# Performance work log

Measured on AMD Instinct MI355X. Metric: run time of the kernel, lower is better.

The kernel has to match this reference:

```python
import jax, jax.numpy as jnp
import numpy as np

N_HEAD = 12
NEG_BIG = 1e10  # additive mask constant from the source


def setup_inputs() -> dict:
    key = jax.random.key(0)
    k1, k2, k3 = jax.random.split(key, 3)
    B, S, D = 8, 1024, 768
    x = jax.random.normal(k1, (B, S, D), dtype=jnp.float32)
    W_attn = jax.random.normal(k2, (D, 3 * D), dtype=jnp.float32) * 0.02
    W_proj = jax.random.normal(k3, (D, D), dtype=jnp.float32) * 0.02
    return {"x": x, "W_attn": W_attn, "W_proj": W_proj}


def reference(x, W_attn, W_proj):
    B, S, D = x.shape
    H = N_HEAD
    dh = D // H  # head dim = 64

    c = x @ W_attn                       # [B, S, 3D]
    q, k, v = jnp.split(c, 3, axis=-1)   # each [B, S, D]

    def split_heads(t):
        return t.reshape(B, S, H, dh).transpose(0, 2, 1, 3)  # [B, H, S, dh]

    q, k, v = split_heads(q), split_heads(k), split_heads(v)

    scale = 1.0 / jnp.sqrt(jnp.asarray(dh, q.dtype))
    a = jnp.einsum('bhqd,bhkd->bhqk', q, k) * scale  # [B, H, S, S]

    # causal mask: i >= j - ns + nd with nd == ns -> lower triangular
    i = jnp.arange(S)[:, None]
    j = jnp.arange(S)[None, :]
    m = (i >= j).astype(a.dtype)  # [S, S]
    a = a * m - (1.0 - m) * NEG_BIG

    a = jax.nn.softmax(a, axis=-1)

    out = jnp.einsum('bhqk,bhkd->bhqd', a, v)        # [B, H, S, dh]
    out = out.transpose(0, 2, 1, 3).reshape(B, S, D)  # merge heads
    return out @ W_proj
```

## Files before the change

### kernel.cpp

```cpp
#include <hip/hip_runtime.h>
#include <hip/hip_bf16.h>

typedef __attribute__((ext_vector_type(4))) float f32x4;
typedef __attribute__((ext_vector_type(8))) short short8;
typedef unsigned short u16;
typedef unsigned int u32;

__device__ __forceinline__ u16 f2bf(float f) {
    u32 u = __float_as_uint(f);
    u32 r = (u + 0x7fffu + ((u >> 16) & 1u)) >> 16;
    return (u16)r;
}
__device__ __forceinline__ u32 pack2bf(float a, float b) {
    __hip_bfloat162 w = __float22bfloat162_rn(float2{a, b});
    return *(u32*)&w;
}
__device__ __forceinline__ void stage16(const u16* gsrc, u16* ldsdst) {
    __builtin_amdgcn_global_load_lds((const __attribute__((address_space(1))) void*)gsrc,
                                     (__attribute__((address_space(3))) void*)ldsdst, 16, 0, 0);
}

__global__ __launch_bounds__(256) void prep(const float* __restrict__ x,
                                            const float* __restrict__ Wa,
                                            const float* __restrict__ Wp,
                                            u16* __restrict__ xb, u16* __restrict__ wat,
                                            u16* __restrict__ wpt) {
    __shared__ float tile[64][65];
    int blk = blockIdx.x;
    if (blk < 576) {
        const float* W;
        u16* Wt;
        int N, bx, by;
        if (blk < 432) {
            W = Wa; Wt = wat; N = 2304; bx = blk % 36; by = blk / 36;
        } else {
            int i = blk - 432;
            W = Wp; Wt = wpt; N = 768; bx = i % 12; by = i / 12;
        }
        int n0 = bx * 64, k0 = by * 64;
        int c = threadIdx.x & 63, r0 = threadIdx.x >> 6;
#pragma unroll
        for (int i = 0; i < 16; ++i) {
            int r = r0 * 16 + i;
            tile[r][c] = W[(size_t)(k0 + r) * N + n0 + c];
        }
        __syncthreads();
#pragma unroll
        for (int i = 0; i < 16; ++i) {
            int r = r0 * 16 + i;
            Wt[(size_t)(n0 + r) * 768 + k0 + c] = f2bf(tile[c][r]);
        }
    } else {
        const int n4 = (8 * 1024 * 768) / 4;
        int i = (blk - 576) * 256 + threadIdx.x;
        int stride = 1024 * 256;
        for (; i < n4; i += stride) {
            float4 v = ((const float4*)x)[i];
            ushort4 o;
            o.x = f2bf(v.x); o.y = f2bf(v.y); o.z = f2bf(v.z); o.w = f2bf(v.w);
            ((ushort4*)xb)[i] = o;
        }
    }
}

template <int MODE, int WM>
__global__ __launch_bounds__(256, 4) void gemmT(const u16* __restrict__ A,
                                                const u16* __restrict__ Bt,
                                                u16* __restrict__ q, u16* __restrict__ kk,
                                                u16* __restrict__ v, float* __restrict__ outf,
                                                int nby) {
    const int K = 768;
    const int BM = 2 * WM;
    __shared__ __align__(16) u16 As[BM * 64];
    __shared__ __align__(16) u16 Bs[128 * 64];
    int nwg = gridDim.x;
    int bid = blockIdx.x;
    int wgid = (bid & 7) * (nwg >> 3) + (bid >> 3);
    int mb = wgid / nby, nb = wgid % nby;
    int m0 = mb * BM, n0 = nb * 128;
    int tid = threadIdx.x;
    int wave = tid >> 6, lane = tid & 63;
    int lo = lane & 15, hi = lane >> 4;
    int wm = (wave >> 1) * WM, wn = (wave & 1) * 64;
    int srow = lane >> 3;
    int schunk = (lane & 7) ^ srow;
    int sw0 = (hi ^ (lo & 7)) * 8;
    int sw1 = ((4 + hi) ^ (lo & 7)) * 8;
    f32x4 acc[WM / 16][4] = {};
    const u16* Ab = A + (size_t)(m0 + (BM / 4) * wave + srow) * K + schunk * 8;
    const u16* Bb = Bt + (size_t)(n0 + 32 * wave + srow) * K + schunk * 8;
    u16* ldsA = &As[((BM / 4) * wave) * 64];
    u16* ldsB = &Bs[(32 * wave) * 64];

    for (int k0 = 0; k0 < K; k0 += 64) {
#pragma unroll
        for (int c = 0; c < BM / 32; ++c)
            stage16(Ab + k0 + (size_t)(8 * c) * K, ldsA + c * 512);
#pragma unroll
        for (int c = 0; c < 4; ++c)
            stage16(Bb + k0 + (size_t)(8 * c) * K, ldsB + c * 512);
        __syncthreads();
#pragma unroll
        for (int ch = 0; ch < 2; ++ch) {
            int sw = ch ? sw1 : sw0;
            short8 af[WM / 16], bf[4];
#pragma unroll
            for (int i = 0; i < WM / 16; ++i)
                af[i] = *(const short8*)&As[(wm + 16 * i + lo) * 64 + sw];
#pragma unroll
            for (int j = 0; j < 4; ++j)
                bf[j] = *(const short8*)&Bs[(wn + 16 * j + lo) * 64 + sw];
#pragma unroll
            for (int i = 0; i < WM / 16; ++i)
#pragma unroll
                for (int j = 0; j < 4; ++j)
                    acc[i][j] = __builtin_amdgcn_mfma_f32_16x16x32_bf16(af[i], bf[j], acc[i][j], 0, 0, 0);
        }
        __syncthreads();
    }

    if (MODE == 0) {
        int ncb = n0 + wn;
        int which = ncb / 768;
        int h = (ncb % 768) >> 6;
        if (which == 2) {
#pragma unroll
            for (int i = 0; i < WM / 16; ++i) {
                int mrow = m0 + wm + 16 * i + 4 * hi;
                int b = mrow >> 10, s0 = mrow & 1023;
                size_t bh = (size_t)(b * 12 + h);
#pragma unroll
                for (int j = 0; j < 4; ++j) {
                    uint2 pk;
                    pk.x = pack2bf(acc[i][j][0], acc[i][j][1]);
                    pk.y = pack2bf(acc[i][j][2], acc[i][j][3]);
                    *(uint2*)&v[(bh * 64 + 16 * j + lo) * 1024 + s0] = pk;
                }
            }
        } else {
            u16* dst = (which == 0) ? q : kk;
            float scale = (which == 0) ? 0.18033688f : 1.0f;
#pragma unroll
            for (int i = 0; i < WM / 16; ++i) {
#pragma unroll
                for (int r = 0; r < 4; ++r) {
                    int mrow = m0 + wm + 16 * i + 4 * hi + r;
                    int b = mrow >> 10, s = mrow & 1023;
                    size_t bh = (size_t)(b * 12 + h);
#pragma unroll
                    for (int j = 0; j < 4; ++j)
                        dst[(bh * 1024 + s) * 64 + 16 * j + lo] = f2bf(acc[i][j][r] * scale);
                }
            }
        }
    } else {
#pragma unroll
        for (int i = 0; i < WM / 16; ++i)
#pragma unroll
            for (int j = 0; j < 4; ++j)
#pragma unroll
                for (int r = 0; r < 4; ++r) {
                    int mrow = m0 + wm + 16 * i + 4 * hi + r;
                    int ncol = n0 + wn + 16 * j + lo;
                    outf[(size_t)mrow * 768 + ncol] = acc[i][j][r];
                }
    }
}

__global__ __launch_bounds__(256) void attn_fwd(const u16* __restrict__ qg,
                                                const u16* __restrict__ kg,
                                                const u16* __restrict__ vg,
                                                u16* __restrict__ ab) {
    __shared__ __align__(16) u16 Kl[2][64 * 64];
    __shared__ __align__(16) u16 Vl[2][64 * 64];
    __shared__ __align__(16) u16 P[4][16][72];
    int tid = threadIdx.x, wave = tid >> 6, lane = tid & 63;
    int lo = lane & 15, hi = lane >> 4;
    int bid = blockIdx.x;
    int j = bid >> 3;
    int bh = (bid & 7) * 12 + (j >> 3);
    int qp = j & 7;
    int b = bh / 12, h = bh % 12;
    u16(*Pw)[72] = P[wave];
    int srow = lane >> 3;
    int schunk = (lane & 7) ^ srow;
    const u16* kA = kg + ((size_t)bh << 16) + (size_t)(16 * wave + srow) * 64 + schunk * 8;
    const u16* vA = vg + ((size_t)bh << 16) + (size_t)(16 * wave + srow) * 1024 + schunk * 8;
    int sw0 = (hi ^ (lo & 7)) * 8;
    int sw1 = ((4 + hi) ^ (lo & 7)) * 8;

    auto stageKV = [&](int bufi, int kv0) {
        u16* kD = Kl[bufi] + wave * 1024;
        u16* vD = Vl[bufi] + wave * 1024;
        stage16(kA + (size_t)kv0 * 64, kD);
        stage16(kA + (size_t)kv0 * 64 + 512, kD + 512);
        stage16(vA + kv0, vD);
        stage16(vA + kv0 + 8 * 1024, vD + 512);
    };

#pragma unroll 1
    for (int part = 0; part < 2; ++part) {
        int qblk = part ? (15 - qp) : qp;
        int q0 = qblk * 64 + 16 * wave;
        const u16* qrow = qg + ((size_t)bh * 1024 + q0 + lo) * 64 + hi * 8;
        short8 qf0 = *(const short8*)qrow;
        short8 qf1 = *(const short8*)(qrow + 32);
        f32x4 acc[4] = {};
        float lsum = 0.f;
        int nt = qblk + 1;
        stageKV(0, 0);
        __syncthreads();
        int cur = 0;
#pragma unroll 1
        for (int t = 0; t < nt; ++t) {
            int kv0 = t * 64;
            if (t + 1 < nt) stageKV(cur ^ 1, kv0 + 64);
            f32x4 st[4] = {};
#pragma unroll
            for (int f = 0; f < 4; ++f) {
                const u16* kp = &Kl[cur][(16 * f + lo) * 64];
                short8 k0 = *(const short8*)(kp + sw0);
                short8 k1 = *(const short8*)(kp + sw1);
                st[f] = __builtin_amdgcn_mfma_f32_16x16x32_bf16(k0, qf0, st[f], 0, 0, 0);
                st[f] = __builtin_amdgcn_mfma_f32_16x16x32_bf16(k1, qf1, st[f], 0, 0, 0);
            }
            if (t == nt - 1) {
#pragma unroll
                for (int f = 0; f < 4; ++f) {
                    int kvb = kv0 + 16 * f + 4 * hi;
#pragma unroll
                    for (int r = 0; r < 4; ++r)
                        if (kvb + r > q0 + lo) st[f][r] = -1e30f;
                }
            }
#pragma unroll
            for (int f = 0; f < 4; ++f) {
                float p0 = exp2f(st[f][0]);
                float p1 = exp2f(st[f][1]);
                float p2 = exp2f(st[f][2]);
                float p3 = exp2f(st[f][3]);
                lsum += (p0 + p1) + (p2 + p3);
                uint2 wv;
                wv.x = pack2bf(p0, p1);
                wv.y = pack2bf(p2, p3);
                *(uint2*)&Pw[lo][16 * f + 4 * hi] = wv;
            }
            asm volatile("s_waitcnt lgkmcnt(0)" ::: "memory");
#pragma unroll
            for (int c = 0; c < 2; ++c) {
                short8 pb = *(const short8*)&Pw[lo][c * 32 + hi * 8];
                int sw = c ? sw1 : sw0;
#pragma unroll
                for (int f2 = 0; f2 < 4; ++f2) {
                    short8 vf = *(const short8*)(&Vl[cur][(16 * f2 + lo) * 64] + sw);
                    acc[f2] = __builtin_amdgcn_mfma_f32_16x16x32_bf16(vf, pb, acc[f2], 0, 0, 0);
                }
            }
            __syncthreads();
            cur ^= 1;
        }
        lsum += __shfl_xor(lsum, 16);
        lsum += __shfl_xor(lsum, 32);
        float inv = 1.0f / lsum;
        u16* orow = ab + ((size_t)b * 1024 + q0 + lo) * 768 + h * 64 + 4 * hi;
#pragma unroll
        for (int f2 = 0; f2 < 4; ++f2) {
            uint2 wv;
            wv.x = pack2bf(acc[f2][0] * inv, acc[f2][1] * inv);
            wv.y = pack2bf(acc[f2][2] * inv, acc[f2][3] * inv);
            *(uint2*)(orow + 16 * f2) = wv;
        }
    }
}

extern "C" void kernel_launch(void* const* d_in, const int* in_sizes, int n_in,
                              void* d_out, int out_size, void* d_ws, size_t ws_size,
                              hipStream_t stream) {
    const float* x = (const float*)d_in[0];
    const float* Wa = (const float*)d_in[1];
    const float* Wp = (const float*)d_in[2];
    float* out = (float*)d_out;
    char* ws = (char*)d_ws;
    const size_t SZ = (size_t)8 * 1024 * 768 * 2;
    u16* xb = (u16*)ws;
    u16* qb = (u16*)(ws + SZ);
    u16* kb = (u16*)(ws + 2 * SZ);
    u16* vb = (u16*)(ws + 3 * SZ);
    u16* ab = (u16*)(ws + 4 * SZ);
    u16* wat = (u16*)(ws + 5 * SZ);
    u16* wpt = (u16*)(ws + 5 * SZ + (size_t)2304 * 768 * 2);

    prep<<<1600, 256, 0, stream>>>(x, Wa, Wp, xb, wat, wpt);
    gemmT<0, 64><<<1152, 256, 0, stream>>>(xb, wat, qb, kb, vb, nullptr, 18);
    attn_fwd<<<768, 256, 0, stream>>>(qb, kb, vb, ab);
    gemmT<1, 32><<<768, 256, 0, stream>>>(ab, wpt, nullptr, nullptr, nullptr, out, 6);
}
```

Baseline: 102.5 us.

## Double-buffer LDS tiles in projection GEMM to overlap loads with MFMA

Adds ping-pong LDS buffers to the bf16 GEMM so the async global-to-LDS loads for the next K tile are issued before computing the current one. Explicit vmcnt waits and barriers replace the two syncthreads per iteration. The goal is to hide global load latency behind MFMA work. In exchange, LDS use doubles and launch bounds drop from 4 to 2 waves-per-EU, which lowers occupancy.

```diff
diff --git a/kernel.cpp b/kernel.cpp
--- a/kernel.cpp
+++ b/kernel.cpp
@@ -64,15 +64,15 @@
 }
 
 template <int MODE, int WM>
-__global__ __launch_bounds__(256, 4) void gemmT(const u16* __restrict__ A,
+__global__ __launch_bounds__(256, 2) void gemmT(const u16* __restrict__ A,
                                                 const u16* __restrict__ Bt,
                                                 u16* __restrict__ q, u16* __restrict__ kk,
                                                 u16* __restrict__ v, float* __restrict__ outf,
                                                 int nby) {
     const int K = 768;
     const int BM = 2 * WM;
-    __shared__ __align__(16) u16 As[BM * 64];
-    __shared__ __align__(16) u16 Bs[128 * 64];
+    __shared__ __align__(16) u16 As[2][BM * 64];
+    __shared__ __align__(16) u16 Bs[2][128 * 64];
     int nwg = gridDim.x;
     int bid = blockIdx.x;
     int wgid = (bid & 7) * (nwg >> 3) + (bid >> 3);
@@ -89,35 +89,54 @@
     f32x4 acc[WM / 16][4] = {};
     const u16* Ab = A + (size_t)(m0 + (BM / 4) * wave + srow) * K + schunk * 8;
     const u16* Bb = Bt + (size_t)(n0 + 32 * wave + srow) * K + schunk * 8;
-    u16* ldsA = &As[((BM / 4) * wave) * 64];
-    u16* ldsB = &Bs[(32 * wave) * 64];
-
-    for (int k0 = 0; k0 < K; k0 += 64) {
+    const int ldsAoff = ((BM / 4) * wave) * 64;
+    const int ldsBoff = (32 * wave) * 64;
+
+    auto stage = [&](int bi, int k0) {
 #pragma unroll
         for (int c = 0; c < BM / 32; ++c)
-            stage16(Ab + k0 + (size_t)(8 * c) * K, ldsA + c * 512);
+            stage16(Ab + k0 + (size_t)(8 * c) * K, &As[bi][ldsAoff + c * 512]);
 #pragma unroll
         for (int c = 0; c < 4; ++c)
-            stage16(Bb + k0 + (size_t)(8 * c) * K, ldsB + c * 512);
-        __syncthreads();
+            stage16(Bb + k0 + (size_t)(8 * c) * K, &Bs[bi][ldsBoff + c * 512]);
+    };
+    auto compute = [&](int bi) {
 #pragma unroll
         for (int ch = 0; ch < 2; ++ch) {
             int sw = ch ? sw1 : sw0;
             short8 af[WM / 16], bf[4];
 #pragma unroll
             for (int i = 0; i < WM / 16; ++i)
-                af[i] = *(const short8*)&As[(wm + 16 * i + lo) * 64 + sw];
+                af[i] = *(const short8*)&As[bi][(wm + 16 * i + lo) * 64 + sw];
 #pragma unroll
             for (int j = 0; j < 4; ++j)
-                bf[j] = *(const short8*)&Bs[(wn + 16 * j + lo) * 64 + sw];
+                bf[j] = *(const short8*)&Bs[bi][(wn + 16 * j + lo) * 64 + sw];
 #pragma unroll
             for (int i = 0; i < WM / 16; ++i)
 #pragma unroll
                 for (int j = 0; j < 4; ++j)
                     acc[i][j] = __builtin_amdgcn_mfma_f32_16x16x32_bf16(af[i], bf[j], acc[i][j], 0, 0, 0);
         }
-        __syncthreads();
+    };
+
+    stage(0, 0);
+    int cur = 0;
+    for (int k0 = 64; k0 < K; k0 += 64) {
+        stage(cur ^ 1, k0);
+        if constexpr (WM == 64)
+            asm volatile("s_waitcnt vmcnt(8)" ::: "memory");
+        else
+            asm volatile("s_waitcnt vmcnt(6)" ::: "memory");
+        __builtin_amdgcn_s_barrier();
+        __builtin_amdgcn_sched_barrier(0);
+        compute(cur);
+        __builtin_amdgcn_sched_barrier(0);
+        __builtin_amdgcn_s_barrier();
+        cur ^= 1;
     }
+    asm volatile("s_waitcnt vmcnt(0)" ::: "memory");
+    __builtin_amdgcn_s_barrier();
+    compute(cur);
 
     if (MODE == 0) {
         int ncb = n0 + wn;
```

Measured after the change: 105.8 us. 1.03x slower.
